# Kernel tuning notes

Measured on AMD Instinct MI355X. Metric: run time of the kernel, lower is better.

Reference implementation:

```python
import jax, jax.numpy as jnp
import numpy as np

B, LQ, LA, D, H = 8, 2048, 2048, 300, 150

def setup_inputs() -> dict:
    key = jax.random.key(0)
    ks = jax.random.split(key, 6)
    return {
        "Q": jax.random.normal(ks[0], (B, LQ, D), dtype=jnp.float32),
        "A": jax.random.normal(ks[1], (B, LA, D), dtype=jnp.float32),
        "Wi": jax.random.normal(ks[2], (D, H), dtype=jnp.float32) * (1.0 / np.sqrt(D)),
        "Wu": jax.random.normal(ks[3], (D, H), dtype=jnp.float32) * (1.0 / np.sqrt(D)),
        "Wg": jax.random.normal(ks[4], (H, H), dtype=jnp.float32) * (1.0 / np.sqrt(H)),
        "Wt": jax.random.normal(ks[5], (2 * H, H), dtype=jnp.float32) * (1.0 / np.sqrt(2 * H)),
        "bi": jnp.zeros((H,), dtype=jnp.float32),
        "bu": jnp.zeros((H,), dtype=jnp.float32),
        "bg": jnp.zeros((H,), dtype=jnp.float32),
        "bt": jnp.zeros((H,), dtype=jnp.float32),
    }

def reference(Q, A, Wi, Wu, Wg, Wt, bi, bu, bg, bt):
    # sigmoid/tanh gated projections (shared weights for Q and A)
    def gate(X):
        return jax.nn.sigmoid(X @ Wi + bi) * jnp.tanh(X @ Wu + bu)
    Qh = gate(Q)  # [B, LQ, H]
    Ah = gate(A)  # [B, LA, H]
    # attention scores G[b,q,a] = <(Qh Wg + bg)[b,q], Ah[b,a]>
    G = jnp.einsum('bqh,bah->bqa', Qh @ Wg + bg, Ah)
    G = jax.nn.softmax(G, axis=1)  # softmax over Q positions
    # H[b,a] = sum_q G[b,q,a] * Qh[b,q]
    Hm = jnp.einsum('bqa,bqh->bah', G, Qh)  # [B, LA, H]
    # 'nn' comparison: relu(concat([Ah, Hm]) @ Wt + bt)
    T = jax.nn.relu(jnp.concatenate([Ah, Hm], axis=-1) @ Wt + bt)
    return T
```

## Files before the change

kernel.cpp:

```cpp
#include <hip/hip_runtime.h>
#include <math.h>

#define BB 8
#define LQ 2048
#define DD 300
#define HHH 150
#define NROWS (BB * LQ)

#define KP 168
#define QTS 72
#define KQ 88
#define WCQ 16384
#define STG_B 32768
#define SLAB_B 46080
#define SLAB_E 23040
#define QHT_OFF_E 11008

typedef __bf16 bf16x8 __attribute__((ext_vector_type(8)));
typedef __bf16 bf16x4 __attribute__((ext_vector_type(4)));
typedef float f32x16 __attribute__((ext_vector_type(16)));

__device__ __forceinline__ void gl_lds16(const void* g, void* l) {
    __builtin_amdgcn_global_load_lds(
        (const __attribute__((address_space(1))) void*)g,
        (__attribute__((address_space(3))) void*)l,
        16, 0, 0);
}
__device__ __forceinline__ void stage_flat(const void* g, void* l, int bytes,
                                           int w, int lane) {
    for (int ofs = w * 1024; ofs < bytes; ofs += 4096)
        gl_lds16((const char*)g + ofs + lane * 16, (char*)l + ofs);
}
__device__ __forceinline__ void stage_flat8(const void* g, void* l, int bytes,
                                            int w, int lane) {
    for (int ofs = w * 1024; ofs < bytes; ofs += 8192)
        gl_lds16((const char*)g + ofs + lane * 16, (char*)l + ofs);
}
__device__ __forceinline__ f32x16 z16() {
    f32x16 v;
#pragma unroll
    for (int i = 0; i < 16; i++) v[i] = 0.f;
    return v;
}
__device__ __forceinline__ bf16x8 cvt8(float4 u, float4 v) {
    return (bf16x8){(__bf16)u.x, (__bf16)u.y, (__bf16)u.z, (__bf16)u.w,
                    (__bf16)v.x, (__bf16)v.y, (__bf16)v.z, (__bf16)v.w};
}
__device__ __forceinline__ unsigned pk2(float lo, float hi) {
    unsigned d;
    asm("v_cvt_pk_bf16_f32 %0, %1, %2" : "=v"(d) : "v"(lo), "v"(hi));
    return d;
}
__device__ __forceinline__ void pl32(unsigned& a, unsigned& b) {
    asm("v_permlane32_swap_b32 %0, %1" : "+v"(a), "+v"(b));
}
__device__ __forceinline__ bf16x8 mk8(unsigned a, unsigned b, unsigned c, unsigned d) {
    union { unsigned u[4]; bf16x8 v; } x;
    x.u[0] = a; x.u[1] = b; x.u[2] = c; x.u[3] = d;
    return x.v;
}

__global__ __launch_bounds__(256) void convert_weights(
    const float* __restrict__ Wi, const float* __restrict__ Wu,
    const float* __restrict__ Wg, const float* __restrict__ Wt,
    __bf16* __restrict__ WiC, __bf16* __restrict__ WuC,
    __bf16* __restrict__ WgT, __bf16* __restrict__ Wt12)
{
    const int z = blockIdx.y;
    const int i = blockIdx.x * 256 + threadIdx.x;
    if (z < 2) {
        if (i >= 4 * WCQ) return;
        int c = i >> 14, rem = i & (WCQ - 1);
        float v = 0.f;
        if (rem < 160 * KQ) {
            int h = rem / KQ, kc = rem - h * KQ;
            int d = c * 80 + kc;
            if (kc < 80 && d < DD && h < HHH) v = (z ? Wu : Wi)[(size_t)d * HHH + h];
        }
        (z ? WuC : WiC)[i] = (__bf16)v;
    } else if (z == 2) {
        if (i >= 2 * WCQ) return;
        int c = i >> 14, rem = i & (WCQ - 1);
        float v = 0.f;
        if (rem < 160 * KQ) {
            int h = rem / KQ, kc = rem - h * KQ;
            int k = c * 80 + kc;
            if (kc < 80 && k < HHH && h < HHH) v = Wg[(size_t)k * HHH + h];
        }
        WgT[i] = (__bf16)v;
    } else {
        if (i >= 2 * 160 * KP) return;
        int c = i / (160 * KP), rem = i - c * (160 * KP);
        int h = rem / KP, kc = rem - h * KP;
        float v = (kc < HHH && h < HHH) ? Wt[(size_t)(c * HHH + kc) * HHH + h] : 0.f;
        Wt12[i] = (__bf16)v;
    }
}

__global__ __launch_bounds__(512, 2) void gatep(
    const float* __restrict__ Q, const float* __restrict__ A,
    const __bf16* __restrict__ WiC, const __bf16* __restrict__ WuC,
    const __bf16* __restrict__ WgT,
    const float* __restrict__ bi, const float* __restrict__ bu,
    const float* __restrict__ bg,
    __bf16* __restrict__ AhB, __bf16* __restrict__ Slab)
{
    __shared__ __align__(16) __bf16 WB[3][WCQ];
    __shared__ __align__(16) __bf16 QhA[128 * KP];
    const int tid = threadIdx.x;
    const int w = tid >> 6, lane = tid & 63;
    const int m32 = lane & 31, half = lane >> 5;
    const int wm = w & 3, wn = w >> 2;
    const int tof = wn ? 3 : 0, tn = wn ? 2 : 3;
    const int z = blockIdx.y;
    const int r0 = blockIdx.x * 128;
    const float* X = z ? A : Q;
    const int lim = z ? 8 : 10;

#define STGP(P)                                                               \
    do {                                                                      \
        const __bf16* _src = ((P) < 8)                                        \
            ? (((P) & 1) ? WuC + ((P) >> 1) * WCQ : WiC + ((P) >> 1) * WCQ)   \
            : WgT + ((P) - 8) * WCQ;                                          \
        stage_flat8(_src, WB[(P) % 3], STG_B, w, lane);                       \
    } while (0)

    STGP(0);
    STGP(1);
    __builtin_amdgcn_sched_barrier(0);

    const float* xrow = X + (size_t)(r0 + wm * 32 + m32) * DD;
    bf16x8 af[4][5];
    const float4 zf = {0.f, 0.f, 0.f, 0.f};
#pragma unroll
    for (int c = 0; c < 4; c++)
#pragma unroll
        for (int ks = 0; ks < 5; ks++) {
            const int colb = c * 80 + ks * 16;
            const int col = colb + half * 8;
            float4 u = zf, v = zf;
            if (colb + 15 < DD) {
                u = *(const float4*)(xrow + col);
                v = *(const float4*)(xrow + col + 4);
            } else if (colb < DD) {
                if (col + 4 <= DD) u = *(const float4*)(xrow + col);
                if (col + 8 <= DD) v = *(const float4*)(xrow + col + 4);
            }
            af[c][ks] = cvt8(u, v);
        }

    f32x16 ai[3], au[3];
#pragma unroll
    for (int t = 0; t < 3; t++) { ai[t] = z16(); au[t] = z16(); }

    __builtin_amdgcn_sched_barrier(0);
    asm volatile("s_waitcnt vmcnt(0)" ::: "memory");
    __builtin_amdgcn_s_barrier();
    __builtin_amdgcn_sched_barrier(0);

#define GPHASE(P, ACC, C)                                                     \
    {                                                                         \
        if ((P) + 2 < lim) { STGP((P) + 2); }                                 \
        const __bf16* Wb = WB[(P) % 3];                                       \
        _Pragma("unroll")                                                     \
        for (int ks = 0; ks < 5; ks++) {                                      \
            _Pragma("unroll")                                                 \
            for (int ti = 0; ti < 3; ti++)                                    \
                if (ti < tn)                                                  \
                    ACC[ti] = __builtin_amdgcn_mfma_f32_32x32x16_bf16(        \
                        af[C][ks],                                            \
                        *(const bf16x8*)(Wb + ((tof + ti) * 32 + m32) * KQ +  \
                                         ks * 16 + half * 8),                 \
                        ACC[ti], 0, 0, 0);                                    \
        }                                                                     \
        __builtin_amdgcn_sched_barrier(0);                                    \
        if ((P) + 2 < lim)                                                    \
            asm volatile("s_waitcnt vmcnt(4)" ::: "memory");                  \
        else                                                                  \
            asm volatile("s_waitcnt vmcnt(0)" ::: "memory");                  \
        __builtin_amdgcn_sched_barrier(0);                                    \
        __builtin_amdgcn_s_barrier();                                         \
        __builtin_amdgcn_sched_barrier(0);                                    \
    }

    GPHASE(0, ai, 0)
    GPHASE(1, au, 0)
    GPHASE(2, ai, 1)
    GPHASE(3, au, 1)
    GPHASE(4, ai, 2)
    GPHASE(5, au, 2)
    GPHASE(6, ai, 3)
    GPHASE(7, au, 3)

#pragma unroll
    for (int ti = 0; ti < 3; ti++) {
        if (ti >= tn) continue;
        int h = (tof + ti) * 32 + m32;
        int hc = h < HHH ? h : 0;
        float bih = bi[hc], buh = bu[hc];
#pragma unroll
        for (int r = 0; r < 16; r++) {
            float v = 0.f;
            if (h < HHH) {
                float xi = ai[ti][r] + bih, xu = au[ti][r] + buh;
                float s = 1.f / (1.f + __expf(-xi));
                float tt = 1.f - 2.f / (1.f + __expf(2.f * xu));
                v = s * tt;
            }
            ai[ti][r] = v;
        }
    }

    if (z) {
#pragma unroll
        for (int ti = 0; ti < 3; ti++) {
            if (ti >= tn) continue;
            int h = (tof + ti) * 32 + m32;
#pragma unroll
            for (int r = 0; r < 16; r++) {
                int rowp = (r & 3) + 8 * (r >> 2) + 4 * half;
                AhB[(size_t)(r0 + wm * 32 + rowp) * KP + h] = (__bf16)ai[ti][r];
            }
        }
        return;
    }

#pragma unroll
    for (int ti = 0; ti < 3; ti++) {
        if (ti >= tn) continue;
        int h = (tof + ti) * 32 + m32;
#pragma unroll
        for (int r = 0; r < 16; r++) {
            int rowp = (r & 3) + 8 * (r >> 2) + 4 * half;
            QhA[(wm * 32 + rowp) * KP + h] = (__bf16)ai[ti][r];
        }
    }
    __syncthreads();

    bf16x8 afq[2][5];
#pragma unroll
    for (int s = 0; s < 2; s++)
#pragma unroll
        for (int ks = 0; ks < 5; ks++)
            afq[s][ks] = *(const bf16x8*)(QhA + (wm * 32 + m32) * KP +
                                          s * 80 + ks * 16 + half * 8);

    f32x16 qg[3];
#pragma unroll
    for (int t = 0; t < 3; t++) qg[t] = z16();
#pragma unroll
    for (int ks = 0; ks < 5; ks++)
#pragma unroll
        for (int ti = 0; ti < 3; ti++)
            if (ti < tn)
                qg[ti] = __builtin_amdgcn_mfma_f32_32x32x16_bf16(
                    afq[0][ks],
                    *(const bf16x8*)(WB[2] + ((tof + ti) * 32 + m32) * KQ + ks * 16 + half * 8),
                    qg[ti], 0, 0, 0);
    __builtin_amdgcn_sched_barrier(0);
    asm volatile("s_waitcnt vmcnt(0)" ::: "memory");
    __builtin_amdgcn_s_barrier();
    __builtin_amdgcn_sched_barrier(0);
#pragma unroll
    for (int ks = 0; ks < 5; ks++)
#pragma unroll
        for (int ti = 0; ti < 3; ti++)
            if (ti < tn)
                qg[ti] = __builtin_amdgcn_mfma_f32_32x32x16_bf16(
                    afq[1][ks],
                    *(const bf16x8*)(WB[0] + ((tof + ti) * 32 + m32) * KQ + ks * 16 + half * 8),
                    qg[ti], 0, 0, 0);

    const int b = r0 >> 11, qt0 = (r0 & 2047) >> 6;
#pragma unroll
    for (int ti = 0; ti < 3; ti++) {
        if (ti >= tn) continue;
        int h = (tof + ti) * 32 + m32;
        int hc = h < HHH ? h : 0;
        float bgh = bg[hc];
#pragma unroll
        for (int r = 0; r < 16; r++) {
            int rowp = (r & 3) + 8 * (r >> 2) + 4 * half;
            int q = (r0 & 2047) + wm * 32 + rowp;
            float v = (h < HHH) ? (qg[ti][r] + bgh) : 0.f;
            Slab[(size_t)(b * 32 + (q >> 6)) * SLAB_E + (q & 63) * KP + h] = (__bf16)v;
        }
    }

    {
        const int jl = tid & 63, tile = (tid >> 6) & 1, hgrp = tid >> 7;
        for (int hseg = hgrp; hseg < 20; hseg += 4) {
            bf16x8 vv = *(const bf16x8*)(QhA + (tile * 64 + jl) * KP + hseg * 8);
            __bf16* dst = Slab + (size_t)(b * 32 + qt0 + tile) * SLAB_E + QHT_OFF_E + jl;
#pragma unroll
            for (int e = 0; e < 8; e++)
                dst[(hseg * 8 + e) * QTS] = vv[e];
        }
    }
}

__global__ __launch_bounds__(512, 2) void attn_mfma(
    const __bf16* __restrict__ Slab, const __bf16* __restrict__ AhB,
    __bf16* __restrict__ O, float* __restrict__ L)
{
    __shared__ __align__(16) __bf16 Buf[3][SLAB_E];
    const int tid = threadIdx.x;
    const int w = tid >> 6, lane = tid & 63;
    const int m32 = lane & 31, half = lane >> 5;
    const int grp = blockIdx.x;
    const int b = grp >> 2, qp = grp & 3;
    const int a0 = blockIdx.y * 256;

    const char* slabBase = (const char*)Slab + (size_t)(b * 32 + qp * 8) * SLAB_B;
    stage_flat8(slabBase, Buf[0], SLAB_B, w, lane);
    __builtin_amdgcn_sched_barrier(0);

    const __bf16* arow = AhB + (size_t)(b * LQ + a0 + w * 32 + m32) * KP + half * 8;
    bf16x8 af[10];
#pragma unroll
    for (int ks = 0; ks < 10; ks++)
        af[ks] = *(const bf16x8*)(arow + ks * 16);
    __builtin_amdgcn_sched_barrier(0);

    stage_flat8(slabBase + SLAB_B, Buf[1], SLAB_B, w, lane);
    __builtin_amdgcn_sched_barrier(0);
    asm volatile("s_waitcnt vmcnt(15)" ::: "memory");
    __builtin_amdgcn_sched_barrier(0);
    __builtin_amdgcn_s_barrier();
    __builtin_amdgcn_sched_barrier(0);

    float lsum = 0.f;
    f32x16 acc[5];
#pragma unroll
    for (int t = 0; t < 5; t++) acc[t] = z16();

    for (int qt = 0; qt < 8; qt++) {
        if (qt < 6)
            stage_flat8(slabBase + (size_t)(qt + 2) * SLAB_B, Buf[(qt + 2) % 3],
                        SLAB_B, w, lane);
        const __bf16* Bq = Buf[qt % 3];
        const __bf16* Bv = Bq + QHT_OFF_E;

        f32x16 s0 = z16(), s1 = z16();
        __builtin_amdgcn_s_setprio(1);
        for (int ks = 0; ks < 10; ks++) {
            bf16x8 b0 = *(const bf16x8*)(Bq + m32 * KP + ks * 16 + half * 8);
            bf16x8 b1 = *(const bf16x8*)(Bq + (32 + m32) * KP + ks * 16 + half * 8);
            s0 = __builtin_amdgcn_mfma_f32_32x32x16_bf16(b0, af[ks], s0, 0, 0, 0);
            s1 = __builtin_amdgcn_mfma_f32_32x32x16_bf16(b1, af[ks], s1, 0, 0, 0);
        }
        __builtin_amdgcn_s_setprio(0);

#pragma unroll
        for (int r = 0; r < 16; r++) { s0[r] = __expf(s0[r]); lsum += s0[r]; }
#pragma unroll
        for (int r = 0; r < 16; r++) { s1[r] = __expf(s1[r]); lsum += s1[r]; }

        bf16x8 pf[4];
        {
            unsigned w01 = pk2(s0[0], s0[1]),   w45 = pk2(s0[4], s0[5]);
            unsigned w23 = pk2(s0[2], s0[3]),   w67 = pk2(s0[6], s0[7]);
            pl32(w01, w45); pl32(w23, w67);
            pf[0] = mk8(w01, w23, w45, w67);
            unsigned x01 = pk2(s0[8], s0[9]),   x45 = pk2(s0[12], s0[13]);
            unsigned x23 = pk2(s0[10], s0[11]), x67 = pk2(s0[14], s0[15]);
            pl32(x01, x45); pl32(x23, x67);
            pf[1] = mk8(x01, x23, x45, x67);
        }
        {
            unsigned w01 = pk2(s1[0], s1[1]),   w45 = pk2(s1[4], s1[5]);
            unsigned w23 = pk2(s1[2], s1[3]),   w67 = pk2(s1[6], s1[7]);
            pl32(w01, w45); pl32(w23, w67);
            pf[2] = mk8(w01, w23, w45, w67);
            unsigned x01 = pk2(s1[8], s1[9]),   x45 = pk2(s1[12], s1[13]);
            unsigned x23 = pk2(s1[10], s1[11]), x67 = pk2(s1[14], s1[15]);
            pl32(x01, x45); pl32(x23, x67);
            pf[3] = mk8(x01, x23, x45, x67);
        }

        __builtin_amdgcn_s_setprio(1);
#pragma unroll
        for (int kk = 0; kk < 4; kk++)
#pragma unroll
            for (int t = 0; t < 5; t++)
                acc[t] = __builtin_amdgcn_mfma_f32_32x32x16_bf16(
                    *(const bf16x8*)(Bv + (t * 32 + m32) * QTS + kk * 16 + half * 8),
                    pf[kk], acc[t], 0, 0, 0);
        __builtin_amdgcn_s_setprio(0);

        if (qt < 7) {
            __builtin_amdgcn_sched_barrier(0);
            if (qt < 6) asm volatile("s_waitcnt vmcnt(5)" ::: "memory");
            else        asm volatile("s_waitcnt vmcnt(0)" ::: "memory");
            __builtin_amdgcn_sched_barrier(0);
            __builtin_amdgcn_s_barrier();
            __builtin_amdgcn_sched_barrier(0);
        }
    }

    float lt = lsum + __shfl_xor(lsum, 32, 64);

    __bf16* Ob = O + ((size_t)qp * NROWS + b * LQ + a0 + w * 32) * 160;
#pragma unroll
    for (int t = 0; t < 5; t++)
#pragma unroll
        for (int rq = 0; rq < 4; rq++) {
            bf16x4 hv = {(__bf16)acc[t][rq * 4 + 0], (__bf16)acc[t][rq * 4 + 1],
                         (__bf16)acc[t][rq * 4 + 2], (__bf16)acc[t][rq * 4 + 3]};
            *(bf16x4*)(Ob + (size_t)m32 * 160 + t * 32 + rq * 8 + half * 4) = hv;
        }
    if (half == 0)
        L[(size_t)qp * NROWS + b * LQ + a0 + w * 32 + m32] = lt;
}

__global__ __launch_bounds__(256, 1) void final_mfma(
    const __bf16* __restrict__ AhB, const __bf16* __restrict__ O,
    const float* __restrict__ L, const __bf16* __restrict__ Wt12,
    const float* __restrict__ bt, float* __restrict__ Out)
{
    __shared__ __align__(16) __bf16 AS[64 * KP];
    __shared__ __align__(16) __bf16 HS[64 * KP];
    __shared__ __align__(16) __bf16 WtS[2 * 160 * KP];
    const int tid = threadIdx.x;
    const int w = tid >> 6, lane = tid & 63;
    const int m32 = lane & 31, half = lane >> 5;
    const int r0 = blockIdx.x * 64;

    stage_flat(AhB + (size_t)r0 * KP, AS, 21504, w, lane);
    stage_flat(Wt12, WtS, 107520, w, lane);

    {
        int rhat = tid >> 2, qq = tid & 3;
        int grow = r0 + rhat;
        float inv = 1.f / (L[grow] + L[NROWS + grow] + L[2 * NROWS + grow] + L[3 * NROWS + grow]);
#pragma unroll
        for (int k = 0; k < 5; k++) {
            float sum[8];
#pragma unroll
            for (int j = 0; j < 8; j++) sum[j] = 0.f;
#pragma unroll
            for (int p = 0; p < 4; p++) {
                bf16x8 x = *(const bf16x8*)(O + ((size_t)p * NROWS + grow) * 160 + qq * 40 + k * 8);
#pragma unroll
                for (int j = 0; j < 8; j++) sum[j] += (float)x[j];
            }
            bf16x8 hv;
#pragma unroll
            for (int j = 0; j < 8; j++) hv[j] = (__bf16)(sum[j] * inv);
            *(bf16x8*)(HS + rhat * KP + qq * 40 + k * 8) = hv;
        }
    }
    __syncthreads();

    const int m = w & 1, th = w >> 1;
    const int tbase = th ? 3 : 0, tn = th ? 2 : 3;
    f32x16 acc[3];
#pragma unroll
    for (int i = 0; i < 3; i++) acc[i] = z16();

    for (int ch = 0; ch < 2; ch++) {
        const __bf16* src = ch ? HS : AS;
        for (int ks = 0; ks < 10; ks++) {
            bf16x8 af = *(const bf16x8*)(src + (m * 32 + m32) * KP + ks * 16 + half * 8);
#pragma unroll
            for (int ti = 0; ti < 3; ti++) {
                if (ti < tn) {
                    int t = tbase + ti;
                    acc[ti] = __builtin_amdgcn_mfma_f32_32x32x16_bf16(
                        af, *(const bf16x8*)(WtS + (ch * 160 + t * 32 + m32) * KP + ks * 16 + half * 8),
                        acc[ti], 0, 0, 0);
                }
            }
        }
    }

#pragma unroll
    for (int ti = 0; ti < 3; ti++) {
        if (ti < tn) {
            int t = tbase + ti;
            int h = t * 32 + m32;
            if (h < HHH) {
                float bth = bt[h];
#pragma unroll
                for (int r = 0; r < 16; r++) {
                    int rowp = (r & 3) + 8 * (r >> 2) + 4 * half;
                    float v = acc[ti][r] + bth;
                    Out[(size_t)(r0 + m * 32 + rowp) * HHH + h] = v > 0.f ? v : 0.f;
                }
            }
        }
    }
}

extern "C" void kernel_launch(void* const* d_in, const int* in_sizes, int n_in,
                              void* d_out, int out_size, void* d_ws, size_t ws_size,
                              hipStream_t stream)
{
    const float* Q  = (const float*)d_in[0];
    const float* A  = (const float*)d_in[1];
    const float* Wi = (const float*)d_in[2];
    const float* Wu = (const float*)d_in[3];
    const float* Wg = (const float*)d_in[4];
    const float* Wt = (const float*)d_in[5];
    const float* bi = (const float*)d_in[6];
    const float* bu = (const float*)d_in[7];
    const float* bg = (const float*)d_in[8];
    const float* bt = (const float*)d_in[9];
    float* out = (float*)d_out;

    char* ws = (char*)d_ws;
    __bf16* Slab = (__bf16*)(ws);
    __bf16* AhB  = (__bf16*)(ws + 11796480);
    __bf16* Op   = (__bf16*)(ws + 17301504);
    float*  Lp   = (float*) (ws + 38273024);
    __bf16* WiC  = (__bf16*)(ws + 38535168);
    __bf16* WuC  = (__bf16*)(ws + 38666240);
    __bf16* WgT  = (__bf16*)(ws + 38797312);
    __bf16* Wt12 = (__bf16*)(ws + 38862848);

    convert_weights<<<dim3(256, 4), 256, 0, stream>>>(Wi, Wu, Wg, Wt,
                                                      WiC, WuC, WgT, Wt12);
    gatep<<<dim3(NROWS / 128, 2), 512, 0, stream>>>(Q, A, WiC, WuC, WgT,
                                                    bi, bu, bg, AhB, Slab);
    attn_mfma<<<dim3(32, 8), 512, 0, stream>>>(Slab, AhB, Op, Lp);
    final_mfma<<<NROWS / 64, 256, 0, stream>>>(AhB, Op, Lp, Wt12, bt, out);
}
```

Measured before the change: 162.6 us.

## Stage gate input rows through LDS and double-buffer weight chunks

The gate kernel now loads each 128-row input tile with coalesced float4 reads by all threads, converts it to bf16 and writes it into a padded LDS buffer. Per-phase A fragments are then read from LDS rather than held as 20 register fragments loaded with strided per-row reads. Weight staging moves from a triple buffer with a two-phase lookahead to a smaller double buffer with a one-phase lookahead and plain __syncthreads. This is meant to cut register pressure and improve global load coalescing, at the cost of extra LDS traffic and less prefetch depth for the weight chunks.

```diff
diff --git a/kernel.cpp b/kernel.cpp
--- a/kernel.cpp
+++ b/kernel.cpp
@@ -11,7 +11,9 @@
 #define QTS 72
 #define KQ 88
 #define WCQ 16384
-#define STG_B 32768
+#define WCE2 14336
+#define STGW_B 28672
+#define XROW 328
 #define SLAB_B 46080
 #define SLAB_E 23040
 #define QHT_OFF_E 11008
@@ -41,10 +43,6 @@
 #pragma unroll
     for (int i = 0; i < 16; i++) v[i] = 0.f;
     return v;
-}
-__device__ __forceinline__ bf16x8 cvt8(float4 u, float4 v) {
-    return (bf16x8){(__bf16)u.x, (__bf16)u.y, (__bf16)u.z, (__bf16)u.w,
-                    (__bf16)v.x, (__bf16)v.y, (__bf16)v.z, (__bf16)v.w};
 }
 __device__ __forceinline__ unsigned pk2(float lo, float hi) {
     unsigned d;
@@ -105,8 +103,8 @@
     const float* __restrict__ bg,
     __bf16* __restrict__ AhB, __bf16* __restrict__ Slab)
 {
-    __shared__ __align__(16) __bf16 WB[3][WCQ];
-    __shared__ __align__(16) __bf16 QhA[128 * KP];
+    __shared__ __align__(16) __bf16 XL[128 * XROW];
+    __shared__ __align__(16) __bf16 WB[2][WCE2];
     const int tid = threadIdx.x;
     const int w = tid >> 6, lane = tid & 63;
     const int m32 = lane & 31, half = lane >> 5;
@@ -117,80 +115,83 @@
     const float* X = z ? A : Q;
     const int lim = z ? 8 : 10;
 
-#define STGP(P)                                                               \
-    do {                                                                      \
-        const __bf16* _src = ((P) < 8)                                        \
-            ? (((P) & 1) ? WuC + ((P) >> 1) * WCQ : WiC + ((P) >> 1) * WCQ)   \
-            : WgT + ((P) - 8) * WCQ;                                          \
-        stage_flat8(_src, WB[(P) % 3], STG_B, w, lane);                       \
-    } while (0)
-
-    STGP(0);
-    STGP(1);
-    __builtin_amdgcn_sched_barrier(0);
-
-    const float* xrow = X + (size_t)(r0 + wm * 32 + m32) * DD;
-    bf16x8 af[4][5];
-    const float4 zf = {0.f, 0.f, 0.f, 0.f};
-#pragma unroll
-    for (int c = 0; c < 4; c++)
-#pragma unroll
-        for (int ks = 0; ks < 5; ks++) {
-            const int colb = c * 80 + ks * 16;
-            const int col = colb + half * 8;
-            float4 u = zf, v = zf;
-            if (colb + 15 < DD) {
-                u = *(const float4*)(xrow + col);
-                v = *(const float4*)(xrow + col + 4);
-            } else if (colb < DD) {
-                if (col + 4 <= DD) u = *(const float4*)(xrow + col);
-                if (col + 8 <= DD) v = *(const float4*)(xrow + col + 4);
-            }
-            af[c][ks] = cvt8(u, v);
-        }
+#define WSRC(P) (((P) < 8) ? (((P) & 1) ? WuC + ((P) >> 1) * WCQ               \
+                                        : WiC + ((P) >> 1) * WCQ)              \
+                           : WgT + ((P) - 8) * WCQ)
+
+    stage_flat8(WSRC(0), WB[0], STGW_B, w, lane);
+
+    {
+        const uint2 zz = {0u, 0u};
+        for (int idx = tid; idx < 128 * 7; idx += 512) {
+            int row = idx / 7, j = idx - row * 7;
+            *(uint2*)((char*)XL + row * 656 + 600 + j * 8) = zz;
+        }
+    }
+
+    {
+        const float4* Xf4 = (const float4*)(X + (size_t)r0 * DD);
+        float4 v[19];
+#pragma unroll
+        for (int i = 0; i < 18; i++) v[i] = Xf4[tid + i * 512];
+        const int jt = tid + 9216;
+        if (jt < 9600) v[18] = Xf4[jt];
+#pragma unroll
+        for (int i = 0; i < 18; i++) {
+            int j = tid + i * 512;
+            int row = j / 75, c4 = j - row * 75;
+            unsigned lo = pk2(v[i].x, v[i].y), hi = pk2(v[i].z, v[i].w);
+            *(uint2*)((char*)XL + row * 656 + c4 * 8) = (uint2){lo, hi};
+        }
+        if (jt < 9600) {
+            int row = jt / 75, c4 = jt - row * 75;
+            unsigned lo = pk2(v[18].x, v[18].y), hi = pk2(v[18].z, v[18].w);
+            *(uint2*)((char*)XL + row * 656 + c4 * 8) = (uint2){lo, hi};
+        }
+    }
 
     f32x16 ai[3], au[3];
 #pragma unroll
     for (int t = 0; t < 3; t++) { ai[t] = z16(); au[t] = z16(); }
 
-    __builtin_amdgcn_sched_barrier(0);
-    asm volatile("s_waitcnt vmcnt(0)" ::: "memory");
-    __builtin_amdgcn_s_barrier();
-    __builtin_amdgcn_sched_barrier(0);
-
-#define GPHASE(P, ACC, C)                                                     \
+    __syncthreads();
+
+    bf16x8 afc[5];
+    const int xrow_off = (wm * 32 + m32) * XROW;
+
+#define GPH2(P, ACC, C, RDAF)                                                 \
     {                                                                         \
-        if ((P) + 2 < lim) { STGP((P) + 2); }                                 \
-        const __bf16* Wb = WB[(P) % 3];                                       \
+        if ((P) + 1 < lim) stage_flat8(WSRC((P) + 1), WB[((P) + 1) & 1],      \
+                                       STGW_B, w, lane);                      \
+        if (RDAF) {                                                           \
+            _Pragma("unroll")                                                 \
+            for (int ks = 0; ks < 5; ks++)                                    \
+                afc[ks] = *(const bf16x8*)(XL + xrow_off + (C) * 80 +         \
+                                           ks * 16 + half * 8);               \
+        }                                                                     \
+        const __bf16* Wb = WB[(P) & 1];                                       \
         _Pragma("unroll")                                                     \
         for (int ks = 0; ks < 5; ks++) {                                      \
             _Pragma("unroll")                                                 \
             for (int ti = 0; ti < 3; ti++)                                    \
                 if (ti < tn)                                                  \
                     ACC[ti] = __builtin_amdgcn_mfma_f32_32x32x16_bf16(        \
-                        af[C][ks],                                            \
+                        afc[ks],                                              \
                         *(const bf16x8*)(Wb + ((tof + ti) * 32 + m32) * KQ +  \
                                          ks * 16 + half * 8),                 \
                         ACC[ti], 0, 0, 0);                                    \
         }                                                                     \
-        __builtin_amdgcn_sched_barrier(0);                                    \
-        if ((P) + 2 < lim)                                                    \
-            asm volatile("s_waitcnt vmcnt(4)" ::: "memory");                  \
-        else                                                                  \
-            asm volatile("s_waitcnt vmcnt(0)" ::: "memory");                  \
-        __builtin_amdgcn_sched_barrier(0);                                    \
-        __builtin_amdgcn_s_barrier();                                         \
-        __builtin_amdgcn_sched_barrier(0);                                    \
-    }
-
-    GPHASE(0, ai, 0)
-    GPHASE(1, au, 0)
-    GPHASE(2, ai, 1)
-    GPHASE(3, au, 1)
-    GPHASE(4, ai, 2)
-    GPHASE(5, au, 2)
-    GPHASE(6, ai, 3)
-    GPHASE(7, au, 3)
+        __syncthreads();                                                      \
+    }
+
+    GPH2(0, ai, 0, 1)
+    GPH2(1, au, 0, 0)
+    GPH2(2, ai, 1, 1)
+    GPH2(3, au, 1, 0)
+    GPH2(4, ai, 2, 1)
+    GPH2(5, au, 2, 0)
+    GPH2(6, ai, 3, 1)
+    GPH2(7, au, 3, 0)
 
 #pragma unroll
     for (int ti = 0; ti < 3; ti++) {
@@ -225,6 +226,7 @@
         return;
     }
 
+    __bf16* QhA = XL;
 #pragma unroll
     for (int ti = 0; ti < 3; ti++) {
         if (ti >= tn) continue;
@@ -236,6 +238,8 @@
         }
     }
     __syncthreads();
+
+    stage_flat8(WSRC(9), WB[1], STGW_B, w, lane);
 
     bf16x8 afq[2][5];
 #pragma unroll
@@ -255,12 +259,9 @@
             if (ti < tn)
                 qg[ti] = __builtin_amdgcn_mfma_f32_32x32x16_bf16(
                     afq[0][ks],
-                    *(const bf16x8*)(WB[2] + ((tof + ti) * 32 + m32) * KQ + ks * 16 + half * 8),
+                    *(const bf16x8*)(WB[0] + ((tof + ti) * 32 + m32) * KQ + ks * 16 + half * 8),
                     qg[ti], 0, 0, 0);
-    __builtin_amdgcn_sched_barrier(0);
-    asm volatile("s_waitcnt vmcnt(0)" ::: "memory");
-    __builtin_amdgcn_s_barrier();
-    __builtin_amdgcn_sched_barrier(0);
+    __syncthreads();
 #pragma unroll
     for (int ks = 0; ks < 5; ks++)
 #pragma unroll
@@ -268,7 +269,7 @@
             if (ti < tn)
                 qg[ti] = __builtin_amdgcn_mfma_f32_32x32x16_bf16(
                     afq[1][ks],
-                    *(const bf16x8*)(WB[0] + ((tof + ti) * 32 + m32) * KQ + ks * 16 + half * 8),
+                    *(const bf16x8*)(WB[1] + ((tof + ti) * 32 + m32) * KQ + ks * 16 + half * 8),
                     qg[ti], 0, 0, 0);
 
     const int b = r0 >> 11, qt0 = (r0 & 2047) >> 6;
```

New measurement: 158.5 us. -2.5%, faster.
